# Kernel optimization log

Measured on AMD Instinct MI355X. Metric: run time of the kernel, lower is better.

The kernel has to match this reference:

```python
import jax, jax.numpy as jnp
import numpy as np
from jax import lax

IN_DIM = 256
MID = IN_DIM // 2          # 128
NUM_FILTERS = 8
OUT_DIM = 256
EMBED_DIM = 256
BN_EPS = 1e-5


def star_relu(x, scale, bias):
    # StarReLU: s * relu(x)**2 + b
    return scale * jnp.square(jax.nn.relu(x)) + bias


def setup_inputs() -> dict:
    key = jax.random.key(0)
    ks = jax.random.split(key, 12)
    B, H, W = 2, 16, 16
    h, w = 128, 128
    inp = {
        "x": jax.random.normal(ks[0], (B, IN_DIM, H, W), jnp.float32),
        "y": jax.random.normal(ks[1], (B, OUT_DIM, h, w), jnp.float32),
        # feature_fuse: 1x1 conv, depthwise 3x3 conv, BatchNorm (eval-mode stats)
        "conv1_w": jax.random.normal(ks[2], (MID, IN_DIM), jnp.float32) * 0.02,
        "conv1_b": jnp.zeros((MID,), jnp.float32),
        "dw_w": jax.random.normal(ks[3], (MID, 3, 3), jnp.float32) * 0.02,
        "dw_b": jnp.zeros((MID,), jnp.float32),
        "bn_gamma": jnp.ones((MID,), jnp.float32),
        "bn_beta": jnp.zeros((MID,), jnp.float32),
        "bn_mean": jax.random.normal(ks[4], (MID,), jnp.float32) * 0.1,
        "bn_var": jax.random.uniform(ks[5], (MID,), jnp.float32, 0.5, 1.5),
        "sr1_scale": jnp.ones((1,), jnp.float32),
        "sr1_bias": jnp.zeros((1,), jnp.float32),
        # channle_expand 1x1 conv
        "ce_w": jax.random.normal(ks[6], (NUM_FILTERS, MID), jnp.float32) * 0.02,
        "ce_b": jnp.zeros((NUM_FILTERS,), jnp.float32),
        "sr2_scale": jnp.ones((1,), jnp.float32),
        "sr2_bias": jnp.zeros((1,), jnp.float32),
        "W_base": jax.random.normal(ks[7], (OUT_DIM * EMBED_DIM, NUM_FILTERS), jnp.float32) * 0.02,
    }
    return inp


def reference(x, y, conv1_w, conv1_b, dw_w, dw_b, bn_gamma, bn_beta, bn_mean,
              bn_var, sr1_scale, sr1_bias, ce_w, ce_b, sr2_scale, sr2_bias, W_base):
    B, _, fh, fw = x.shape
    b, c, h, w = y.shape
    ph, pw = h // fh, w // fw

    # feature_fuse
    t = jnp.einsum('bchw,oc->bohw', x, conv1_w) + conv1_b[None, :, None, None]
    t = lax.conv_general_dilated(
        t, dw_w[:, None, :, :], (1, 1), ((1, 1), (1, 1)),
        feature_group_count=MID,
        dimension_numbers=('NCHW', 'OIHW', 'NCHW')) + dw_b[None, :, None, None]
    t = bn_gamma[None, :, None, None] * (t - bn_mean[None, :, None, None]) \
        * lax.rsqrt(bn_var + BN_EPS)[None, :, None, None] + bn_beta[None, :, None, None]
    t = star_relu(t, sr1_scale, sr1_bias)

    # channle_expand + act -> per-location filter coefficients [b, F, fh, fw]
    wdec = star_relu(jnp.einsum('bchw,fc->bfhw', t, ce_w) + ce_b[None, :, None, None],
                     sr2_scale, sr2_bias)

    # hypernetwork: [b, E*O, fh, fw], flattened as (embed_dim, out_dim)
    Wd = jnp.einsum('bfhw,ef->behw', wdec, W_base)
    Wd = Wd.reshape(b, EMBED_DIM, OUT_DIM, fh, fw)

    # massive-group 1x1 conv == per-(batch, block) small GEMM over spatial patches
    yb = y.reshape(b, c, fh, ph, fw, pw)
    out = jnp.einsum('beoij,boipjq->beipjq', Wd, yb)  # [b, E, fh, ph, fw, pw]
    return out.reshape(b, EMBED_DIM, h, w)
```

## Files before the change

### kernel.cpp

```cpp
#include <hip/hip_runtime.h>
#include <stdint.h>

typedef unsigned short u16t;
typedef unsigned int   u32t;
typedef _Float16       h16;
typedef __attribute__((ext_vector_type(2))) _Float16 h16x2;
typedef __attribute__((ext_vector_type(8))) short    short8;
typedef __attribute__((ext_vector_type(4))) float    f32x4;

#if defined(__has_builtin)
#if __has_builtin(__builtin_amdgcn_fdot2)
#define HAVE_DOT2 1
#endif
#endif

__device__ __forceinline__ float dot2h(u32t a, u32t b, float c){
#ifdef HAVE_DOT2
  return __builtin_amdgcn_fdot2(__builtin_bit_cast(h16x2, a),
                                __builtin_bit_cast(h16x2, b), c, false);
#else
  h16x2 ha = __builtin_bit_cast(h16x2, a), hb = __builtin_bit_cast(h16x2, b);
  return c + (float)ha[0]*(float)hb[0] + (float)ha[1]*(float)hb[1];
#endif
}

__device__ __forceinline__ float bf2f(u16t h){
  union { u32t u; float f; } c; c.u = ((u32t)h) << 16; return c.f;
}
__device__ __forceinline__ u32t pk2bf(float a, float b){
  u32t ua = __builtin_bit_cast(u32t, a) + 0x8000u;
  u32t ub = __builtin_bit_cast(u32t, b) + 0x8000u;
  return __builtin_amdgcn_perm(ub, ua, 0x07060302u);
}
__device__ __forceinline__ u32t pk2h(float a, float b){
  h16x2 h = { (h16)a, (h16)b };
  return __builtin_bit_cast(u32t, h);
}

template<bool BF>
__device__ __forceinline__ float ldv(const void* p, size_t i){
  if constexpr (BF) return bf2f(((const u16t*)p)[i]);
  else              return ((const float*)p)[i];
}
template<bool BF>
__device__ __forceinline__ void ld8(const void* p, size_t i, float* v){
  if constexpr (BF){
    uint4 u = *(const uint4*)((const u16t*)p + i);
    const u32t a[4] = {u.x, u.y, u.z, u.w};
#pragma unroll
    for (int d = 0; d < 4; ++d){
      v[2*d]   = bf2f((u16t)(a[d] & 0xffffu));
      v[2*d+1] = bf2f((u16t)(a[d] >> 16));
    }
  } else {
    const float4* q = (const float4*)((const float*)p + i);
    float4 A = q[0], B = q[1];
    v[0]=A.x; v[1]=A.y; v[2]=A.z; v[3]=A.w;
    v[4]=B.x; v[5]=B.y; v[6]=B.z; v[7]=B.w;
  }
}

__device__ __forceinline__ bool probe_bf(const void* xv){
  const u16t* p = (const u16t*)xv;
  const int lane = threadIdx.x & 63;
  const u16t h0 = p[lane], h1 = p[lane + 64];
  const int e0 = (h0 >> 7) & 0xff, e1 = (h1 >> 7) & 0xff;
  unsigned long long b0 = __ballot(e0 >= 90 && e0 <= 150);
  unsigned long long b1 = __ballot(e1 >= 90 && e1 <= 150);
  return (__popcll(b0) + __popcll(b1)) >= 104;
}

template<bool BF>
__device__ __forceinline__ void pre12_body(
    const void* x, const void* w, const void* bias,
    const void* dww, const void* dwb,
    const void* bng, const void* bnb, const void* bnm, const void* bnv,
    const void* s1s, const void* s1b, float* t2, float (*ts)[256], int bq)
{
  const int b = bq >> 5, cq = bq & 31;
  const int cl = threadIdx.x >> 8, ij = threadIdx.x & 255;
  const int c = cq * 4 + cl;
  const int i = ij >> 4, j = ij & 15;
  float a0 = ldv<BF>(bias, c);
  const size_t xb = (size_t)b * 65536 + ij;
#pragma unroll 8
  for (int k = 0; k < 256; ++k)
    a0 += ldv<BF>(x, xb + (size_t)k * 256) * ldv<BF>(w, (size_t)c * 256 + k);
  ts[cl][ij] = a0;
  __syncthreads();
  float s = ldv<BF>(dwb, c);
#pragma unroll
  for (int di = 0; di < 3; ++di){
    const int ii = i + di - 1;
    if (ii < 0 || ii > 15) continue;
#pragma unroll
    for (int dj = 0; dj < 3; ++dj){
      const int jj = j + dj - 1;
      if (jj < 0 || jj > 15) continue;
      s += ts[cl][ii * 16 + jj] * ldv<BF>(dww, c * 9 + di * 3 + dj);
    }
  }
  const float v = ldv<BF>(bng, c) * (s - ldv<BF>(bnm, c)) *
                  rsqrtf(ldv<BF>(bnv, c) + 1e-5f) + ldv<BF>(bnb, c);
  const float r = fmaxf(v, 0.0f);
  t2[((size_t)b * 128 + c) * 256 + ij] = ldv<BF>(s1s, 0) * r * r + ldv<BF>(s1b, 0);
}

template<bool BF>
__device__ __forceinline__ void prew_body(const void* wb, uint4* wbh2, int pb){
  const int t = pb * 1024 + threadIdx.x;
  const int e = t & 255, o = t >> 8;
  float v[8];
  ld8<BF>(wb, ((size_t)e * 256 + o) * 8, v);
  wbh2[(size_t)o * 256 + e] = make_uint4(pk2h(v[0], v[1]), pk2h(v[2], v[3]),
                                         pk2h(v[4], v[5]), pk2h(v[6], v[7]));
}

__global__ __launch_bounds__(1024) void k_fused(
    const void* x,
    const void* w1, const void* b1, const void* dww, const void* dwb,
    const void* bng, const void* bnb, const void* bnm, const void* bnv,
    const void* s1s, const void* s1b, const void* wb,
    float* t2, uint4* wbh2)
{
  __shared__ float ts[4][256];
  const bool bf = probe_bf(x);
  const int bid = blockIdx.x;
  if (bid < 64){
    if (bf) pre12_body<true >(x,w1,b1,dww,dwb,bng,bnb,bnm,bnv,s1s,s1b,t2,ts,bid);
    else    pre12_body<false>(x,w1,b1,dww,dwb,bng,bnb,bnm,bnv,s1s,s1b,t2,ts,bid);
  } else {
    if (bf) prew_body<true >(wb, wbh2, bid - 64);
    else    prew_body<false>(wb, wbh2, bid - 64);
  }
}

template<bool BF>
__device__ __forceinline__ void main_body(
    const void* y, const float* t2, const void* cew, const void* ceb,
    const void* s2s, const void* s2b,
    const uint4* wbh2, float* out, u16t* smem)
{
  const int bid = blockIdx.x;
  const int b = bid >> 7, i = (bid >> 3) & 15, jp = bid & 7, j0 = jp * 2;
  const int tid = threadIdx.x;
  const int wv = tid >> 6, lane = tid & 63;

  {
    const int w4 = tid & 3, p = (tid >> 2) & 7, opq = tid >> 5;
    u32t pk[4][4];
#pragma unroll
    for (int r = 0; r < 4; ++r){
      const int o = (r * 32 + opq) * 2;
      const size_t base = (((size_t)(b * 256 + o) * 128) + i * 8 + p) * 128
                        + jp * 16 + w4 * 4;
      if constexpr (BF){
        const u16t* yp = (const u16t*)y;
        const uint2 u0 = *(const uint2*)(yp + base);
        const uint2 u1 = *(const uint2*)(yp + base + 16384);
        pk[r][0] = (u0.x & 0xffffu) | (u1.x << 16);
        pk[r][1] = (u0.x >> 16)     | (u1.x & 0xffff0000u);
        pk[r][2] = (u0.y & 0xffffu) | (u1.y << 16);
        pk[r][3] = (u0.y >> 16)     | (u1.y & 0xffff0000u);
      } else {
        const float* yp = (const float*)y;
        const float4 A = *(const float4*)(yp + base);
        const float4 B = *(const float4*)(yp + base + 16384);
        pk[r][0] = pk2bf(A.x, B.x); pk[r][1] = pk2bf(A.y, B.y);
        pk[r][2] = pk2bf(A.z, B.z); pk[r][3] = pk2bf(A.w, B.w);
      }
    }
#pragma unroll
    for (int r = 0; r < 4; ++r){
      const int o  = (r * 32 + opq) * 2;
      const int oc = o >> 3, osub = o & 7;
#pragma unroll
      for (int k = 0; k < 4; ++k){
        const int w_l  = w4 * 4 + k;
        const int row  = (w_l >> 3) * 64 + p * 8 + (w_l & 7);
        const int phys = (oc + row) & 31;
        *(u32t*)(smem + row * 256 + phys * 8 + osub) = pk[r][k];
      }
    }
  }

  float* wds = (float*)(smem + 32768);

  if (tid < 64){
    const int g = (tid >> 5) & 1, f = (tid >> 2) & 7, cq = tid & 3;
    const int ij = i * 16 + j0 + g;
    const float* tp = t2 + (size_t)b * 32768 + ij;
    float a = 0.0f;
#pragma unroll 8
    for (int c = cq; c < 128; c += 4)
      a += tp[(size_t)c * 256] * ldv<BF>(cew, (size_t)f * 128 + c);
    a += __shfl_xor(a, 1);
    a += __shfl_xor(a, 2);
    if (cq == 0){
      const float tot = a + ldv<BF>(ceb, f);
      const float rr  = fmaxf(tot, 0.0f);
      wds[g * 8 + f] = ldv<BF>(s2s, 0) * rr * rr + ldv<BF>(s2b, 0);
    }
  }

  const int l15 = lane & 15, l4 = lane >> 4;
  const int e0  = wv * 16;

  const uint4* wrow = wbh2 + (size_t)(l4 * 8) * 256 + e0 + l15;

  uint4 Wb[2][8];
#pragma unroll
  for (int r = 0; r < 8; ++r) Wb[0][r] = wrow[(size_t)r * 256];

  f32x4 acc[2][4];
#pragma unroll
  for (int g = 0; g < 2; ++g)
#pragma unroll
    for (int nt = 0; nt < 4; ++nt)
      acc[g][nt] = (f32x4){0.f, 0.f, 0.f, 0.f};

  __syncthreads();

  u32t wdp[2][4];
#pragma unroll
  for (int g = 0; g < 2; ++g)
#pragma unroll
    for (int d = 0; d < 4; ++d)
      wdp[g][d] = pk2h(wds[g * 8 + 2 * d], wds[g * 8 + 2 * d + 1]);

#pragma unroll
  for (int ks = 0; ks < 8; ++ks){
    const int cur = ks & 1;
    if (ks < 7){
#pragma unroll
      for (int r = 0; r < 8; ++r)
        Wb[cur ^ 1][r] = wrow[(size_t)((ks + 1) * 32 + r) * 256];
    }
    float s[2][8];
#pragma unroll
    for (int r = 0; r < 8; ++r){
      const uint4 w4 = Wb[cur][r];
#pragma unroll
      for (int g = 0; g < 2; ++g){
        float t = dot2h(w4.x, wdp[g][0], 0.0f);
        t = dot2h(w4.y, wdp[g][1], t);
        t = dot2h(w4.z, wdp[g][2], t);
        s[g][r] = dot2h(w4.w, wdp[g][3], t);
      }
    }
#pragma unroll
    for (int g = 0; g < 2; ++g){
      u32t a4[4];
#pragma unroll
      for (int d = 0; d < 4; ++d) a4[d] = pk2bf(s[g][2*d], s[g][2*d+1]);
      const short8 af = __builtin_bit_cast(short8, *(uint4*)a4);
#pragma unroll
      for (int nt = 0; nt < 4; ++nt){
        const int row  = g * 64 + nt * 16 + l15;
        const int phys = (ks * 4 + l4 + row) & 31;
        const short8 bfr = *(const short8*)(smem + row * 256 + phys * 8);
        acc[g][nt] = __builtin_amdgcn_mfma_f32_16x16x32_bf16(af, bfr, acc[g][nt], 0, 0, 0);
      }
    }
  }

#pragma unroll
  for (int g = 0; g < 2; ++g){
#pragma unroll
    for (int nt = 0; nt < 4; ++nt){
      const int col = nt * 16 + l15;
      const int pp = col >> 3, qq = col & 7;
#pragma unroll
      for (int r = 0; r < 4; ++r){
        const int ee = e0 + l4 * 4 + r;
        const size_t oaddr = ((size_t)(b * 256 + ee) * 128 + (i * 8 + pp)) * 128
                           + (j0 + g) * 8 + qq;
        out[oaddr] = acc[g][nt][r];
      }
    }
  }
}
__global__ __launch_bounds__(1024, 2) void k_main(
    const void* x, const void* y, const float* t2, const void* cew, const void* ceb,
    const void* s2s, const void* s2b,
    const uint4* wbh2, float* out)
{
  extern __shared__ __align__(16) u16t smem[];
  if (probe_bf(x)) main_body<true >(y, t2, cew, ceb, s2s, s2b, wbh2, out, smem);
  else             main_body<false>(y, t2, cew, ceb, s2s, s2b, wbh2, out, smem);
}

extern "C" void kernel_launch(void* const* d_in, const int* in_sizes, int n_in,
                              void* d_out, int out_size, void* d_ws, size_t ws_size,
                              hipStream_t stream)
{
  float* t2    = (float*)d_ws;
  uint4* wbh2  = (uint4*)((char*)d_ws + 262144);

  k_fused<<<dim3(128), dim3(1024), 0, stream>>>(
      d_in[0], d_in[2], d_in[3], d_in[4], d_in[5], d_in[6], d_in[7],
      d_in[8], d_in[9], d_in[10], d_in[11], d_in[16], t2, wbh2);

  const int lds_bytes = 65536 + 64;
  hipFuncSetAttribute((const void*)k_main,
                      hipFuncAttributeMaxDynamicSharedMemorySize, lds_bytes);
  k_main<<<dim3(256), dim3(1024), lds_bytes, stream>>>(
      d_in[0], d_in[1], t2, d_in[12], d_in[13], d_in[14], d_in[15],
      wbh2, (float*)d_out);
}
```

Measured before the change: 155.9 us.

## Pipeline y-tile staging into shared memory in chunks overlapped with MFMA compute

The y tile is now loaded and written to shared memory in four output-channel chunks with a two-deep register buffer, so MFMA work on earlier chunks overlaps global loads of later ones. Previously the whole tile was staged before any compute began. The W_base register double-buffer is dropped in favour of per-step loads, and the launch bound is raised to hint at more resident blocks, which caps registers per thread. This adds a barrier per chunk and risks spills or exposed W_base load latency.

```diff
diff --git a/kernel.cpp b/kernel.cpp
--- a/kernel.cpp
+++ b/kernel.cpp
@@ -146,43 +146,55 @@
   const int tid = threadIdx.x;
   const int wv = tid >> 6, lane = tid & 63;
 
-  {
-    const int w4 = tid & 3, p = (tid >> 2) & 7, opq = tid >> 5;
-    u32t pk[4][4];
-#pragma unroll
-    for (int r = 0; r < 4; ++r){
-      const int o = (r * 32 + opq) * 2;
-      const size_t base = (((size_t)(b * 256 + o) * 128) + i * 8 + p) * 128
-                        + jp * 16 + w4 * 4;
-      if constexpr (BF){
-        const u16t* yp = (const u16t*)y;
-        const uint2 u0 = *(const uint2*)(yp + base);
-        const uint2 u1 = *(const uint2*)(yp + base + 16384);
-        pk[r][0] = (u0.x & 0xffffu) | (u1.x << 16);
-        pk[r][1] = (u0.x >> 16)     | (u1.x & 0xffff0000u);
-        pk[r][2] = (u0.y & 0xffffu) | (u1.y << 16);
-        pk[r][3] = (u0.y >> 16)     | (u1.y & 0xffff0000u);
-      } else {
-        const float* yp = (const float*)y;
-        const float4 A = *(const float4*)(yp + base);
-        const float4 B = *(const float4*)(yp + base + 16384);
-        pk[r][0] = pk2bf(A.x, B.x); pk[r][1] = pk2bf(A.y, B.y);
-        pk[r][2] = pk2bf(A.z, B.z); pk[r][3] = pk2bf(A.w, B.w);
+  const int w4 = tid & 3, p = (tid >> 2) & 7, opq = tid >> 5;
+
+  float fA[2][4], fB[2][4];
+  u32t  uA[2][2], uB[2][2];
+
+  auto issue_loads = [&](int cs, int buf){
+    const int o = (cs * 32 + opq) * 2;
+    const size_t base = (((size_t)(b * 256 + o) * 128) + i * 8 + p) * 128
+                      + jp * 16 + w4 * 4;
+    if constexpr (BF){
+      const u16t* yp = (const u16t*)y;
+      const uint2 u0 = *(const uint2*)(yp + base);
+      const uint2 u1 = *(const uint2*)(yp + base + 16384);
+      uA[buf][0] = u0.x; uA[buf][1] = u0.y;
+      uB[buf][0] = u1.x; uB[buf][1] = u1.y;
+    } else {
+      const float* yp = (const float*)y;
+      const float4 A = *(const float4*)(yp + base);
+      const float4 B = *(const float4*)(yp + base + 16384);
+      fA[buf][0]=A.x; fA[buf][1]=A.y; fA[buf][2]=A.z; fA[buf][3]=A.w;
+      fB[buf][0]=B.x; fB[buf][1]=B.y; fB[buf][2]=B.z; fB[buf][3]=B.w;
+    }
+  };
+  auto write_chunk = [&](int cs, int buf){
+    u32t pk[4];
+    if constexpr (BF){
+#pragma unroll
+      for (int d = 0; d < 2; ++d){
+        const u32t lo = uA[buf][d], hi = uB[buf][d];
+        pk[2*d]   = (lo & 0xffffu) | (hi << 16);
+        pk[2*d+1] = (lo >> 16)     | (hi & 0xffff0000u);
       }
-    }
-#pragma unroll
-    for (int r = 0; r < 4; ++r){
-      const int o  = (r * 32 + opq) * 2;
-      const int oc = o >> 3, osub = o & 7;
-#pragma unroll
-      for (int k = 0; k < 4; ++k){
-        const int w_l  = w4 * 4 + k;
-        const int row  = (w_l >> 3) * 64 + p * 8 + (w_l & 7);
-        const int phys = (oc + row) & 31;
-        *(u32t*)(smem + row * 256 + phys * 8 + osub) = pk[r][k];
-      }
-    }
-  }
+    } else {
+#pragma unroll
+      for (int k = 0; k < 4; ++k) pk[k] = pk2bf(fA[buf][k], fB[buf][k]);
+    }
+    const int o  = (cs * 32 + opq) * 2;
+    const int oc = o >> 3, osub = o & 7;
+#pragma unroll
+    for (int k = 0; k < 4; ++k){
+      const int w_l  = w4 * 4 + k;
+      const int row  = (w_l >> 3) * 64 + p * 8 + (w_l & 7);
+      const int phys = (oc + row) & 31;
+      *(u32t*)(smem + row * 256 + phys * 8 + osub) = pk[k];
+    }
+  };
+
+  issue_loads(0, 0);
+  issue_loads(1, 1);
 
   float* wds = (float*)(smem + 32768);
 
@@ -203,15 +215,13 @@
     }
   }
 
+  write_chunk(0, 0);
+
   const int l15 = lane & 15, l4 = lane >> 4;
   const int e0  = wv * 16;
 
   const uint4* wrow = wbh2 + (size_t)(l4 * 8) * 256 + e0 + l15;
 
-  uint4 Wb[2][8];
-#pragma unroll
-  for (int r = 0; r < 8; ++r) Wb[0][r] = wrow[(size_t)r * 256];
-
   f32x4 acc[2][4];
 #pragma unroll
   for (int g = 0; g < 2; ++g)
@@ -219,47 +229,52 @@
     for (int nt = 0; nt < 4; ++nt)
       acc[g][nt] = (f32x4){0.f, 0.f, 0.f, 0.f};
 
-  __syncthreads();
-
   u32t wdp[2][4];
-#pragma unroll
-  for (int g = 0; g < 2; ++g)
-#pragma unroll
-    for (int d = 0; d < 4; ++d)
-      wdp[g][d] = pk2h(wds[g * 8 + 2 * d], wds[g * 8 + 2 * d + 1]);
-
-#pragma unroll
-  for (int ks = 0; ks < 8; ++ks){
-    const int cur = ks & 1;
-    if (ks < 7){
-#pragma unroll
-      for (int r = 0; r < 8; ++r)
-        Wb[cur ^ 1][r] = wrow[(size_t)((ks + 1) * 32 + r) * 256];
-    }
-    float s[2][8];
-#pragma unroll
-    for (int r = 0; r < 8; ++r){
-      const uint4 w4 = Wb[cur][r];
+
+#pragma unroll
+  for (int cs = 0; cs < 4; ++cs){
+    __syncthreads();
+    if (cs == 0){
+#pragma unroll
+      for (int g = 0; g < 2; ++g)
+#pragma unroll
+        for (int d = 0; d < 4; ++d)
+          wdp[g][d] = pk2h(wds[g * 8 + 2 * d], wds[g * 8 + 2 * d + 1]);
+    }
+    if (cs + 2 <= 3) issue_loads(cs + 2, cs & 1);
+    if (cs + 1 <= 3) write_chunk(cs + 1, (cs + 1) & 1);
+
+#pragma unroll
+    for (int kh = 0; kh < 2; ++kh){
+      const int ks = cs * 2 + kh;
+      uint4 Wb[8];
+#pragma unroll
+      for (int r = 0; r < 8; ++r) Wb[r] = wrow[(size_t)(ks * 32 + r) * 256];
+      float s[2][8];
+#pragma unroll
+      for (int r = 0; r < 8; ++r){
+        const uint4 w4r = Wb[r];
+#pragma unroll
+        for (int g = 0; g < 2; ++g){
+          float t = dot2h(w4r.x, wdp[g][0], 0.0f);
+          t = dot2h(w4r.y, wdp[g][1], t);
+          t = dot2h(w4r.z, wdp[g][2], t);
+          s[g][r] = dot2h(w4r.w, wdp[g][3], t);
+        }
+      }
 #pragma unroll
       for (int g = 0; g < 2; ++g){
-        float t = dot2h(w4.x, wdp[g][0], 0.0f);
-        t = dot2h(w4.y, wdp[g][1], t);
-        t = dot2h(w4.z, wdp[g][2], t);
-        s[g][r] = dot2h(w4.w, wdp[g][3], t);
-      }
-    }
-#pragma unroll
-    for (int g = 0; g < 2; ++g){
-      u32t a4[4];
-#pragma unroll
-      for (int d = 0; d < 4; ++d) a4[d] = pk2bf(s[g][2*d], s[g][2*d+1]);
-      const short8 af = __builtin_bit_cast(short8, *(uint4*)a4);
-#pragma unroll
-      for (int nt = 0; nt < 4; ++nt){
-        const int row  = g * 64 + nt * 16 + l15;
-        const int phys = (ks * 4 + l4 + row) & 31;
-        const short8 bfr = *(const short8*)(smem + row * 256 + phys * 8);
-        acc[g][nt] = __builtin_amdgcn_mfma_f32_16x16x32_bf16(af, bfr, acc[g][nt], 0, 0, 0);
+        u32t a4[4];
+#pragma unroll
+        for (int d = 0; d < 4; ++d) a4[d] = pk2bf(s[g][2*d], s[g][2*d+1]);
+        const short8 af = __builtin_bit_cast(short8, *(uint4*)a4);
+#pragma unroll
+        for (int nt = 0; nt < 4; ++nt){
+          const int row  = g * 64 + nt * 16 + l15;
+          const int phys = (ks * 4 + l4 + row) & 31;
+          const short8 bfr = *(const short8*)(smem + row * 256 + phys * 8);
+          acc[g][nt] = __builtin_amdgcn_mfma_f32_16x16x32_bf16(af, bfr, acc[g][nt], 0, 0, 0);
+        }
       }
     }
   }
@@ -280,7 +295,7 @@
     }
   }
 }
-__global__ __launch_bounds__(1024, 2) void k_main(
+__global__ __launch_bounds__(1024, 4) void k_main(
     const void* x, const void* y, const float* t2, const void* cew, const void* ceb,
     const void* s2s, const void* s2b,
     const uint4* wbh2, float* out)
```

Result: no change. 154.6 us (-0.8%).
